# Kernel optimization log

Hardware: AMD Instinct MI355X
Metric: run time of the kernel (lower is better)

The kernel has to match this reference:

```python
import jax, jax.numpy as jnp
import numpy as np

B = 2048

def _conv(x, w, b, stride):
    y = jax.lax.conv_general_dilated(x, w, (stride, stride), 'VALID',
                                     dimension_numbers=('NCHW', 'OIHW', 'NCHW'))
    return y + b[None, :, None, None]

def _local_conv(x, w, b):
    # w: (Ho, Wo, Co, Ci, kh, kw), b: (Ho, Wo, Co); stride 1, valid
    Ho, Wo, Co, Ci, kh, kw = w.shape
    # patches: (B, Ci, kh*kw, Ho, Wo) -- sliding windows, small fixed loop over kernel taps
    patches = jnp.stack([x[:, :, i:i + Ho, j:j + Wo]
                         for i in range(kh) for j in range(kw)], axis=2)
    wf = w.reshape(Ho, Wo, Co, Ci, kh * kw)
    y = jnp.einsum('bcphw,hwocp->bohw', patches, wf)
    return y + jnp.transpose(b, (2, 0, 1))[None]

def setup_inputs() -> dict:
    key = jax.random.key(0)
    ks = jax.random.split(key, 18)
    s = 0.05
    inp = {
        'x': jax.random.normal(ks[0], (B, 5, 60, 60), dtype=jnp.float32),
        'info': jax.random.normal(ks[1], (B, 8), dtype=jnp.float32),
        'w1': jax.random.normal(ks[2], (32, 5, 3, 3), dtype=jnp.float32) * s,
        'b1': jnp.zeros((32,), dtype=jnp.float32),
        'w2a': jax.random.normal(ks[3], (64, 32, 3, 3), dtype=jnp.float32) * s,
        'b2a': jnp.zeros((64,), dtype=jnp.float32),
        'w2b': jax.random.normal(ks[4], (64, 64, 3, 3), dtype=jnp.float32) * s,
        'b2b': jnp.zeros((64,), dtype=jnp.float32),
        'lw3': jax.random.normal(ks[5], (9, 9, 64, 64, 5, 5), dtype=jnp.float32) * s,
        'lb3': jnp.zeros((9, 9, 64), dtype=jnp.float32),
        'lw4': jax.random.normal(ks[6], (5, 5, 64, 64, 5, 5), dtype=jnp.float32) * s,
        'lb4': jnp.zeros((5, 5, 64), dtype=jnp.float32),
        'lw5': jax.random.normal(ks[7], (3, 3, 64, 64, 3, 3), dtype=jnp.float32) * s,
        'lb5': jnp.zeros((3, 3, 64), dtype=jnp.float32),
        'hw': jax.random.normal(ks[8], (2, 584), dtype=jnp.float32) * s,
        'hb': jnp.zeros((2,), dtype=jnp.float32),
    }
    return inp

def reference(x, info, w1, b1, w2a, b2a, w2b, b2b, lw3, lb3, lw4, lb4, lw5, lb5, hw, hb):
    h = jnp.tanh(_conv(x, w1, b1, 2))            # (B,32,29,29)
    h = jnp.tanh(_conv(h, w2a, b2a, 1))          # (B,64,27,27)
    h = jnp.tanh(_conv(h, w2b, b2b, 2))          # (B,64,13,13)
    h = jnp.tanh(_local_conv(h, lw3, lb3))       # (B,64,9,9)
    h = jnp.tanh(_local_conv(h, lw4, lb4))       # (B,64,5,5)
    h = jnp.tanh(_local_conv(h, lw5, lb5))       # (B,64,3,3)
    h = h.reshape(h.shape[0], -1)                # (B,576)
    h = jnp.concatenate([h, info], axis=1)       # (B,584)
    logits = h @ hw.T + hb                       # (B,2)
    return jax.nn.softmax(logits, axis=1)
```

## Files before the change

### kernel.cpp

```cpp
#include <hip/hip_runtime.h>
#include <stdint.h>

#define THREADS 256

typedef short bf16x8 __attribute__((ext_vector_type(8)));
typedef float f32x4 __attribute__((ext_vector_type(4)));
typedef unsigned uint2_ __attribute__((ext_vector_type(2)));

__device__ __forceinline__ unsigned short f2bf(float v) {
  unsigned u = __builtin_bit_cast(unsigned, v);
  u = (u + 0x7fff + ((u >> 16) & 1)) >> 16;
  return (unsigned short)u;
}
__device__ __forceinline__ float bf2f(unsigned short h) {
  return __builtin_bit_cast(float, (unsigned)h << 16);
}
__device__ __forceinline__ float fast_tanh(float x) {
  return 1.f - 2.f / (__expf(2.f * x) + 1.f);
}

__device__ __forceinline__ int xcd_swizzle(int wg, int nwg) {
  const int q = nwg >> 3, rr = nwg & 7;
  const int xcd = wg & 7, l = wg >> 3;
  return (xcd < rr ? xcd * (q + 1) : rr * (q + 1) + (xcd - rr) * q) + l;
}

__global__ void pack_w1t(const float* __restrict__ w1, float* __restrict__ w1t) {
  int idx = blockIdx.x * THREADS + threadIdx.x;
  if (idx >= 45 * 32) return;
  int t = idx >> 5, co = idx & 31;
  w1t[t * 32 + co] = w1[co * 45 + t];
}

__global__ void __launch_bounds__(256) conv1_direct(
    const float* __restrict__ x, const float* __restrict__ w1t,
    const float* __restrict__ bias, unsigned short* __restrict__ out, int Bc,
    int bstart) {
  constexpr int CI = 5, CO = 32, IH = 60, IW = 60, OH = 29, OW = 29;
  constexpr int RPB = 2, NRB = 15;

  __shared__ float xs[CI * 5 * 60];

  const int tid = threadIdx.x;
  const int b = blockIdx.x / NRB;
  const int qb = blockIdx.x % NRB;
  const int oh0 = qb * RPB;
  const int rows = min(RPB, OH - oh0);
  const int ih0 = oh0 * 2;
  const int ihn = rows * 2 + 1;

  const float* xp = x + (size_t)(bstart + b) * (CI * IH * IW);

  const int nf4 = CI * ihn * 15;
  for (int i = tid; i < nf4; i += 256) {
    int col = i % 15;
    int row = i / 15;
    int ci = row / ihn, r = row % ihn;
    ((float4*)xs)[row * 15 + col] = ((const float4*)xp)[(ci * IH + ih0 + r) * 15 + col];
  }
  __syncthreads();

  const int lane = tid & 63;
  const int wu = __builtin_amdgcn_readfirstlane(tid >> 6);
  if (lane >= rows * OW) return;
  const int r = lane / OW, c = lane % OW;
  const int base = (r * 2) * 60 + c * 2;
  const int cstr = ihn * 60;

  float acc[8];
#pragma unroll
  for (int j = 0; j < 8; j++) acc[j] = bias[wu * 8 + j];

#pragma unroll
  for (int ci = 0; ci < CI; ci++)
#pragma unroll
    for (int kh = 0; kh < 3; kh++)
#pragma unroll
      for (int kw = 0; kw < 3; kw++) {
        const float v = xs[ci * cstr + base + kh * 60 + kw];
        const float* wt = w1t + ((ci * 3 + kh) * 3 + kw) * 32 + wu * 8;
#pragma unroll
        for (int j = 0; j < 8; j++) acc[j] = fmaf(v, wt[j], acc[j]);
      }

  const int p = (oh0 + r) * OW + c;
  bf16x8 o;
#pragma unroll
  for (int j = 0; j < 8; j++) o[j] = (short)f2bf(fast_tanh(acc[j]));
  *(bf16x8*)(out + ((size_t)p * Bc + b) * CO + wu * 8) = o;
}

template <int CI, int KS>
__global__ void __launch_bounds__(THREADS) pack_w(const float* __restrict__ w,
                                                  unsigned short* __restrict__ wp,
                                                  int npos) {
  constexpr int K = CI * KS * KS;
  constexpr int S = K / 32;
  int idx = blockIdx.x * THREADS + threadIdx.x;
  int total = npos * S * 2048;
  if (idx >= total) return;
  int e = idx & 7;
  int lane = (idx >> 3) & 63;
  int mt = (idx >> 9) & 3;
  int rest = idx >> 11;
  int s = rest % S, pos = rest / S;
  int co = mt * 16 + (lane & 15);
  int k = s * 32 + (lane >> 4) * 8 + e;
  int tap = k / CI, ci = k % CI;
  int kh = tap / KS, kw = tap % KS;
  float v = w[((((size_t)pos * 64 + co) * CI + ci) * KS + kh) * KS + kw];
  wp[idx] = f2bf(v);
}

template <int CI, int IH, int IW, int OH, int OW, int KS, int ST, bool LOCAL, int BW>
__global__ void __launch_bounds__(256) conv_mfma(
    const unsigned short* __restrict__ X, const unsigned short* __restrict__ Wp,
    const float* __restrict__ bias, unsigned short* __restrict__ Y, int Bc) {
  constexpr int S = CI * KS * KS / 32;
  constexpr int NPOS = OH * OW;
  constexpr int CW = 4 / BW;
  constexpr int MT = 4 / CW;

  const int tid = threadIdx.x;
  const int lane = tid & 63;
  const int wu = tid >> 6;
  const int n = lane & 15, g = lane >> 4;
  const int bw = wu % BW, cw = wu / BW;

  const int nbt = Bc / (BW * 64);
  int wg = xcd_swizzle(blockIdx.x, gridDim.x);
  int pos, btile;
  if (LOCAL) {
    btile = wg % nbt;
    pos = wg / nbt;
  } else {
    pos = wg % NPOS;
    btile = wg / NPOS;
  }
  const int oh = pos / OW, ow = pos % OW;
  const int b0 = btile * (BW * 64) + bw * 64;
  const int bA = b0 + n;

  const unsigned short* Wpp = Wp + (LOCAL ? (size_t)pos * (S * 2048) : 0);

  f32x4 acc[MT][4] = {};

#pragma unroll 2
  for (int s = 0; s < S; s++) {
    const int tap = (s * 32) / CI;
    const int ci0 = (s * 32) % CI + g * 8;
    const int kh = tap / KS, kw = tap % KS;
    const int pin = (oh * ST + kh) * IW + (ow * ST + kw);
    const unsigned short* xb = X + ((size_t)pin * Bc + bA) * CI + ci0;

    bf16x8 bfr[4];
#pragma unroll
    for (int j = 0; j < 4; j++) bfr[j] = *(const bf16x8*)(xb + j * 16 * CI);

    bf16x8 af[MT];
#pragma unroll
    for (int mt = 0; mt < MT; mt++)
      af[mt] =
          *(const bf16x8*)(Wpp + ((size_t)((s * 4 + cw * MT + mt) * 64 + lane) << 3));

#pragma unroll
    for (int mt = 0; mt < MT; mt++)
#pragma unroll
      for (int j = 0; j < 4; j++)
        acc[mt][j] =
            __builtin_amdgcn_mfma_f32_16x16x32_bf16(af[mt], bfr[j], acc[mt][j], 0, 0, 0);
  }

#pragma unroll
  for (int mt = 0; mt < MT; mt++) {
#pragma unroll
    for (int j = 0; j < 4; j++) {
      unsigned short o[4];
#pragma unroll
      for (int r = 0; r < 4; r++) {
        const int co = (cw * MT + mt) * 16 + g * 4 + r;
        o[r] = f2bf(fast_tanh(acc[mt][j][r] +
                              (LOCAL ? bias[pos * 64 + co] : bias[co])));
      }
      const int b = b0 + j * 16 + n;
      uint2_ pk;
      pk[0] = (unsigned)o[0] | ((unsigned)o[1] << 16);
      pk[1] = (unsigned)o[2] | ((unsigned)o[3] << 16);
      *(uint2_*)(Y + ((size_t)pos * Bc + b) * 64 + (cw * MT + mt) * 16 + g * 4) = pk;
    }
  }
}

__global__ void head_k(const unsigned short* __restrict__ h5,
                       const float* __restrict__ info, const float* __restrict__ hw,
                       const float* __restrict__ hb, float* __restrict__ out, int Bc,
                       int bstart) {
  int b = blockIdx.x * THREADS + threadIdx.x;
  if (b >= Bc) return;
  float l0 = hb[0], l1 = hb[1];
  for (int pos = 0; pos < 9; pos++) {
#pragma unroll
    for (int cb = 0; cb < 8; cb++) {
      bf16x8 v8 = *(const bf16x8*)(h5 + ((size_t)pos * Bc + b) * 64 + cb * 8);
#pragma unroll
      for (int j = 0; j < 8; j++) {
        float v = bf2f((unsigned short)v8[j]);
        int f = (cb * 8 + j) * 9 + pos;
        l0 = fmaf(v, hw[f], l0);
        l1 = fmaf(v, hw[584 + f], l1);
      }
    }
  }
#pragma unroll
  for (int k = 0; k < 8; k++) {
    float v = info[(size_t)(bstart + b) * 8 + k];
    l0 = fmaf(v, hw[576 + k], l0);
    l1 = fmaf(v, hw[584 + 576 + k], l1);
  }
  float m = fmaxf(l0, l1);
  float e0 = __expf(l0 - m), e1 = __expf(l1 - m);
  float s = e0 + e1;
  out[(size_t)(bstart + b) * 2 + 0] = e0 / s;
  out[(size_t)(bstart + b) * 2 + 1] = e1 / s;
}


extern "C" void kernel_launch(void* const* d_in, const int* in_sizes, int n_in,
                              void* d_out, int out_size, void* d_ws, size_t ws_size,
                              hipStream_t stream) {
  const float* x = (const float*)d_in[0];
  const float* info = (const float*)d_in[1];
  const float* w1 = (const float*)d_in[2];
  const float* b1 = (const float*)d_in[3];
  const float* w2a = (const float*)d_in[4];
  const float* b2a = (const float*)d_in[5];
  const float* w2b = (const float*)d_in[6];
  const float* b2b = (const float*)d_in[7];
  const float* lw3 = (const float*)d_in[8];
  const float* lb3 = (const float*)d_in[9];
  const float* lw4 = (const float*)d_in[10];
  const float* lb4 = (const float*)d_in[11];
  const float* lw5 = (const float*)d_in[12];
  const float* lb5 = (const float*)d_in[13];
  const float* hw = (const float*)d_in[14];
  const float* hb = (const float*)d_in[15];
  float* out = (float*)d_out;

  const int B = in_sizes[0] / 18000;

  const size_t SZ2A = 9ull * 2048, SZ2B = 18ull * 2048, SZ3 = 81ull * 50 * 2048,
               SZ4 = 25ull * 50 * 2048, SZ5 = 9ull * 18 * 2048;
  unsigned short* wp2a = (unsigned short*)d_ws;
  unsigned short* wp2b = wp2a + SZ2A;
  unsigned short* wp3 = wp2b + SZ2B;
  unsigned short* wp4 = wp3 + SZ3;
  unsigned short* wp5 = wp4 + SZ4;
  size_t wp_bytes = (SZ2A + SZ2B + SZ3 + SZ4 + SZ5) * 2;
  wp_bytes = (wp_bytes + 255) & ~(size_t)255;
  float* w1t = (float*)((char*)d_ws + wp_bytes);
  size_t w1t_bytes = ((45 * 32 * 4) + 255) & ~(size_t)255;

  const size_t PSA = 53824, PSB = 93312;
  const size_t per_sample = PSA + PSB;
  int Bc = B;
  while (Bc > 256 && wp_bytes + w1t_bytes + (size_t)Bc * per_sample + 4096 > ws_size)
    Bc >>= 1;

  char* base = (char*)d_ws + wp_bytes + w1t_bytes;
  unsigned short* bufA = (unsigned short*)base;
  unsigned short* bufB = (unsigned short*)(base + (size_t)Bc * PSA);

  hipLaunchKernelGGL(pack_w1t, dim3(6), dim3(THREADS), 0, stream, w1, w1t);
  hipLaunchKernelGGL((pack_w<32, 3>), dim3((SZ2A + 255) / 256), dim3(THREADS), 0, stream,
                     w2a, wp2a, 1);
  hipLaunchKernelGGL((pack_w<64, 3>), dim3((SZ2B + 255) / 256), dim3(THREADS), 0, stream,
                     w2b, wp2b, 1);
  hipLaunchKernelGGL((pack_w<64, 5>), dim3((SZ3 + 255) / 256), dim3(THREADS), 0, stream,
                     lw3, wp3, 81);
  hipLaunchKernelGGL((pack_w<64, 5>), dim3((SZ4 + 255) / 256), dim3(THREADS), 0, stream,
                     lw4, wp4, 25);
  hipLaunchKernelGGL((pack_w<64, 3>), dim3((SZ5 + 255) / 256), dim3(THREADS), 0, stream,
                     lw5, wp5, 9);

  const int nchunks = B / Bc;
  for (int c = 0; c < nchunks; c++) {
    const int bstart = c * Bc;

    hipLaunchKernelGGL(conv1_direct, dim3(Bc * 15), dim3(256), 0, stream, x, w1t, b1,
                       bufA, Bc, bstart);
    hipLaunchKernelGGL((conv_mfma<32, 29, 29, 27, 27, 3, 1, false, 4>),
                       dim3(729 * (Bc / 256)), dim3(256), 0, stream, bufA, wp2a, b2a,
                       bufB, Bc);
    hipLaunchKernelGGL((conv_mfma<64, 27, 27, 13, 13, 3, 2, false, 4>),
                       dim3(169 * (Bc / 256)), dim3(256), 0, stream, bufB, wp2b, b2b,
                       bufA, Bc);
    hipLaunchKernelGGL((conv_mfma<64, 13, 13, 9, 9, 5, 1, true, 4>),
                       dim3(81 * (Bc / 256)), dim3(256), 0, stream, bufA, wp3, lb3, bufB,
                       Bc);
    hipLaunchKernelGGL((conv_mfma<64, 9, 9, 5, 5, 5, 1, true, 2>),
                       dim3(25 * (Bc / 128)), dim3(256), 0, stream, bufB, wp4, lb4, bufA,
                       Bc);
    hipLaunchKernelGGL((conv_mfma<64, 5, 5, 3, 3, 3, 1, true, 1>),
                       dim3(9 * (Bc / 64)), dim3(256), 0, stream, bufA, wp5, lb5, bufB,
                       Bc);
    hipLaunchKernelGGL(head_k, dim3((Bc + THREADS - 1) / THREADS), dim3(THREADS), 0,
                       stream, bufB, info, hw, hb, out, Bc, bstart);
  }
}
```

Baseline: 640.7 us.

## Retile MFMA conv warp tiles and double-buffer fragment loads across K steps

Generalises the conv_mfma warp tile to MT=BW co-tiles by NJ batch subtiles, and retunes per-layer tiles. Dense convs use 2x8 tiles per wave (more reuse of weights across batch) and the local convs use smaller batch tiles, which gives more workgroups. The K loop now prefetches the next step's A/B fragments into a second register set before issuing MFMAs on the current one, overlapping global loads with compute. This raises register pressure, and the smaller local-conv tiles reload weights more often.

```diff
diff --git a/kernel.cpp b/kernel.cpp
--- a/kernel.cpp
+++ b/kernel.cpp
@@ -112,14 +112,15 @@
   wp[idx] = f2bf(v);
 }
 
-template <int CI, int IH, int IW, int OH, int OW, int KS, int ST, bool LOCAL, int BW>
+template <int CI, int IH, int IW, int OH, int OW, int KS, int ST, bool LOCAL, int BW,
+          int NJ>
 __global__ void __launch_bounds__(256) conv_mfma(
     const unsigned short* __restrict__ X, const unsigned short* __restrict__ Wp,
     const float* __restrict__ bias, unsigned short* __restrict__ Y, int Bc) {
   constexpr int S = CI * KS * KS / 32;
   constexpr int NPOS = OH * OW;
-  constexpr int CW = 4 / BW;
-  constexpr int MT = 4 / CW;
+  constexpr int MT = BW;
+  constexpr int BPB = BW * NJ * 16;
 
   const int tid = threadIdx.x;
   const int lane = tid & 63;
@@ -127,7 +128,7 @@
   const int n = lane & 15, g = lane >> 4;
   const int bw = wu % BW, cw = wu / BW;
 
-  const int nbt = Bc / (BW * 64);
+  const int nbt = Bc / BPB;
   int wg = xcd_swizzle(blockIdx.x, gridDim.x);
   int pos, btile;
   if (LOCAL) {
@@ -138,43 +139,48 @@
     btile = wg / NPOS;
   }
   const int oh = pos / OW, ow = pos % OW;
-  const int b0 = btile * (BW * 64) + bw * 64;
+  const int b0 = btile * BPB + bw * (NJ * 16);
   const int bA = b0 + n;
 
   const unsigned short* Wpp = Wp + (LOCAL ? (size_t)pos * (S * 2048) : 0);
 
-  f32x4 acc[MT][4] = {};
-
-#pragma unroll 2
-  for (int s = 0; s < S; s++) {
+  auto LD = [&](int s, bf16x8* af, bf16x8* bf) {
     const int tap = (s * 32) / CI;
     const int ci0 = (s * 32) % CI + g * 8;
     const int kh = tap / KS, kw = tap % KS;
     const int pin = (oh * ST + kh) * IW + (ow * ST + kw);
     const unsigned short* xb = X + ((size_t)pin * Bc + bA) * CI + ci0;
-
-    bf16x8 bfr[4];
-#pragma unroll
-    for (int j = 0; j < 4; j++) bfr[j] = *(const bf16x8*)(xb + j * 16 * CI);
-
-    bf16x8 af[MT];
+#pragma unroll
+    for (int j = 0; j < NJ; j++) bf[j] = *(const bf16x8*)(xb + j * 16 * CI);
 #pragma unroll
     for (int mt = 0; mt < MT; mt++)
       af[mt] =
           *(const bf16x8*)(Wpp + ((size_t)((s * 4 + cw * MT + mt) * 64 + lane) << 3));
-
+  };
+
+  f32x4 acc[MT][NJ] = {};
+  auto MM = [&](bf16x8* af, bf16x8* bf) {
 #pragma unroll
     for (int mt = 0; mt < MT; mt++)
 #pragma unroll
-      for (int j = 0; j < 4; j++)
+      for (int j = 0; j < NJ; j++)
         acc[mt][j] =
-            __builtin_amdgcn_mfma_f32_16x16x32_bf16(af[mt], bfr[j], acc[mt][j], 0, 0, 0);
+            __builtin_amdgcn_mfma_f32_16x16x32_bf16(af[mt], bf[j], acc[mt][j], 0, 0, 0);
+  };
+
+  bf16x8 afA[MT], bfA[NJ], afB[MT], bfB[NJ];
+  LD(0, afA, bfA);
+  for (int s = 0; s < S; s += 2) {
+    if (s + 1 < S) LD(s + 1, afB, bfB);
+    MM(afA, bfA);
+    if (s + 2 < S) LD(s + 2, afA, bfA);
+    if (s + 1 < S) MM(afB, bfB);
   }
 
 #pragma unroll
   for (int mt = 0; mt < MT; mt++) {
 #pragma unroll
-    for (int j = 0; j < 4; j++) {
+    for (int j = 0; j < NJ; j++) {
       unsigned short o[4];
 #pragma unroll
       for (int r = 0; r < 4; r++) {
@@ -288,20 +294,20 @@
 
     hipLaunchKernelGGL(conv1_direct, dim3(Bc * 15), dim3(256), 0, stream, x, w1t, b1,
                        bufA, Bc, bstart);
-    hipLaunchKernelGGL((conv_mfma<32, 29, 29, 27, 27, 3, 1, false, 4>),
+    hipLaunchKernelGGL((conv_mfma<32, 29, 29, 27, 27, 3, 1, false, 2, 8>),
                        dim3(729 * (Bc / 256)), dim3(256), 0, stream, bufA, wp2a, b2a,
                        bufB, Bc);
-    hipLaunchKernelGGL((conv_mfma<64, 27, 27, 13, 13, 3, 2, false, 4>),
+    hipLaunchKernelGGL((conv_mfma<64, 27, 27, 13, 13, 3, 2, false, 2, 8>),
                        dim3(169 * (Bc / 256)), dim3(256), 0, stream, bufB, wp2b, b2b,
                        bufA, Bc);
-    hipLaunchKernelGGL((conv_mfma<64, 13, 13, 9, 9, 5, 1, true, 4>),
-                       dim3(81 * (Bc / 256)), dim3(256), 0, stream, bufA, wp3, lb3, bufB,
+    hipLaunchKernelGGL((conv_mfma<64, 13, 13, 9, 9, 5, 1, true, 2, 4>),
+                       dim3(81 * (Bc / 128)), dim3(256), 0, stream, bufA, wp3, lb3, bufB,
                        Bc);
-    hipLaunchKernelGGL((conv_mfma<64, 9, 9, 5, 5, 5, 1, true, 2>),
-                       dim3(25 * (Bc / 128)), dim3(256), 0, stream, bufB, wp4, lb4, bufA,
+    hipLaunchKernelGGL((conv_mfma<64, 9, 9, 5, 5, 5, 1, true, 1, 4>),
+                       dim3(25 * (Bc / 64)), dim3(256), 0, stream, bufB, wp4, lb4, bufA,
                        Bc);
-    hipLaunchKernelGGL((conv_mfma<64, 5, 5, 3, 3, 3, 1, true, 1>),
-                       dim3(9 * (Bc / 64)), dim3(256), 0, stream, bufA, wp5, lb5, bufB,
+    hipLaunchKernelGGL((conv_mfma<64, 5, 5, 3, 3, 3, 1, true, 1, 2>),
+                       dim3(9 * (Bc / 32)), dim3(256), 0, stream, bufA, wp5, lb5, bufB,
                        Bc);
     hipLaunchKernelGGL(head_k, dim3((Bc + THREADS - 1) / THREADS), dim3(THREADS), 0,
                        stream, bufB, info, hw, hb, out, Bc, bstart);
```

Measured after the change: 737.0 us. +15.0%, slower.

## Stage conv MFMA operands through double-buffered LDS with async global-to-LDS loads

Applied to the files above, without the earlier changes.

The MFMA conv kernel now stages each K-slice of packed weights and activations into shared memory using global_load_lds, double-buffered so the next slice loads while the current one is multiplied. Every wave now covers all 64 output channels over its own batch sub-tile, so weights are fetched once per block instead of per wave. The last local conv now uses 128-sample tiles. The change adds one barrier per K step and more LDS use, and the 16-byte global_load_lds width depends on hardware support.

```diff
diff --git a/kernel.cpp b/kernel.cpp
--- a/kernel.cpp
+++ b/kernel.cpp
@@ -6,6 +6,9 @@
 typedef short bf16x8 __attribute__((ext_vector_type(8)));
 typedef float f32x4 __attribute__((ext_vector_type(4)));
 typedef unsigned uint2_ __attribute__((ext_vector_type(2)));
+
+#define GPTR(x) ((const __attribute__((address_space(1))) void*)(x))
+#define LPTR(x) ((__attribute__((address_space(3))) void*)(x))
 
 __device__ __forceinline__ unsigned short f2bf(float v) {
   unsigned u = __builtin_bit_cast(unsigned, v);
@@ -112,22 +115,24 @@
   wp[idx] = f2bf(v);
 }
 
-template <int CI, int IH, int IW, int OH, int OW, int KS, int ST, bool LOCAL, int BW>
+template <int CI, int IH, int IW, int OH, int OW, int KS, int ST, bool LOCAL, int BT>
 __global__ void __launch_bounds__(256) conv_mfma(
     const unsigned short* __restrict__ X, const unsigned short* __restrict__ Wp,
     const float* __restrict__ bias, unsigned short* __restrict__ Y, int Bc) {
   constexpr int S = CI * KS * KS / 32;
   constexpr int NPOS = OH * OW;
-  constexpr int CW = 4 / BW;
-  constexpr int MT = 4 / CW;
+  constexpr int NJ = BT / 64;
+  constexpr int NB = BT / 64;
+
+  __shared__ unsigned short As[2][2048];
+  __shared__ unsigned short Bs[2][BT * 32];
 
   const int tid = threadIdx.x;
   const int lane = tid & 63;
   const int wu = tid >> 6;
   const int n = lane & 15, g = lane >> 4;
-  const int bw = wu % BW, cw = wu / BW;
-
-  const int nbt = Bc / (BW * 64);
+
+  const int nbt = Bc / BT;
   int wg = xcd_swizzle(blockIdx.x, gridDim.x);
   int pos, btile;
   if (LOCAL) {
@@ -138,55 +143,72 @@
     btile = wg / NPOS;
   }
   const int oh = pos / OW, ow = pos % OW;
-  const int b0 = btile * (BW * 64) + bw * 64;
-  const int bA = b0 + n;
+  const int b0 = btile * BT;
 
   const unsigned short* Wpp = Wp + (LOCAL ? (size_t)pos * (S * 2048) : 0);
 
-  f32x4 acc[MT][4] = {};
-
-#pragma unroll 2
-  for (int s = 0; s < S; s++) {
+  const int srow = tid >> 2;
+  const int scol = (tid & 3) * 8;
+
+  auto stage = [&](int s, int buf) {
+    __builtin_amdgcn_global_load_lds(GPTR(Wpp + s * 2048 + tid * 8),
+                                     LPTR(&As[buf][tid * 8]), 16, 0, 0);
     const int tap = (s * 32) / CI;
-    const int ci0 = (s * 32) % CI + g * 8;
+    const int ci0 = (s * 32) % CI;
     const int kh = tap / KS, kw = tap % KS;
     const int pin = (oh * ST + kh) * IW + (ow * ST + kw);
-    const unsigned short* xb = X + ((size_t)pin * Bc + bA) * CI + ci0;
-
-    bf16x8 bfr[4];
-#pragma unroll
-    for (int j = 0; j < 4; j++) bfr[j] = *(const bf16x8*)(xb + j * 16 * CI);
-
-    bf16x8 af[MT];
-#pragma unroll
-    for (int mt = 0; mt < MT; mt++)
-      af[mt] =
-          *(const bf16x8*)(Wpp + ((size_t)((s * 4 + cw * MT + mt) * 64 + lane) << 3));
-
-#pragma unroll
-    for (int mt = 0; mt < MT; mt++)
-#pragma unroll
-      for (int j = 0; j < 4; j++)
+    const size_t base = (size_t)pin * Bc + b0;
+#pragma unroll
+    for (int i = 0; i < NB; i++)
+      __builtin_amdgcn_global_load_lds(
+          GPTR(X + (base + i * 64 + srow) * CI + ci0 + scol),
+          LPTR(&Bs[buf][i * 2048 + tid * 8]), 16, 0, 0);
+  };
+
+  f32x4 acc[4][NJ] = {};
+
+  stage(0, 0);
+  int buf = 0;
+  for (int s = 0; s < S; s++) {
+    __syncthreads();
+    if (s + 1 < S) stage(s + 1, buf ^ 1);
+
+    bf16x8 bfr[NJ];
+#pragma unroll
+    for (int j = 0; j < NJ; j++) {
+      const int local_b = wu * (NJ * 16) + j * 16 + n;
+      bfr[j] = *(const bf16x8*)(&Bs[buf][local_b * 32 + g * 8]);
+    }
+    bf16x8 af[4];
+#pragma unroll
+    for (int mt = 0; mt < 4; mt++)
+      af[mt] = *(const bf16x8*)(&As[buf][(mt * 64 + lane) * 8]);
+
+#pragma unroll
+    for (int mt = 0; mt < 4; mt++)
+#pragma unroll
+      for (int j = 0; j < NJ; j++)
         acc[mt][j] =
             __builtin_amdgcn_mfma_f32_16x16x32_bf16(af[mt], bfr[j], acc[mt][j], 0, 0, 0);
-  }
-
-#pragma unroll
-  for (int mt = 0; mt < MT; mt++) {
-#pragma unroll
-    for (int j = 0; j < 4; j++) {
+    buf ^= 1;
+  }
+
+#pragma unroll
+  for (int mt = 0; mt < 4; mt++) {
+#pragma unroll
+    for (int j = 0; j < NJ; j++) {
       unsigned short o[4];
 #pragma unroll
       for (int r = 0; r < 4; r++) {
-        const int co = (cw * MT + mt) * 16 + g * 4 + r;
+        const int co = mt * 16 + g * 4 + r;
         o[r] = f2bf(fast_tanh(acc[mt][j][r] +
                               (LOCAL ? bias[pos * 64 + co] : bias[co])));
       }
-      const int b = b0 + j * 16 + n;
+      const int b = b0 + wu * (NJ * 16) + j * 16 + n;
       uint2_ pk;
       pk[0] = (unsigned)o[0] | ((unsigned)o[1] << 16);
       pk[1] = (unsigned)o[2] | ((unsigned)o[3] << 16);
-      *(uint2_*)(Y + ((size_t)pos * Bc + b) * 64 + (cw * MT + mt) * 16 + g * 4) = pk;
+      *(uint2_*)(Y + ((size_t)pos * Bc + b) * 64 + mt * 16 + g * 4) = pk;
     }
   }
 }
@@ -288,20 +310,20 @@
 
     hipLaunchKernelGGL(conv1_direct, dim3(Bc * 15), dim3(256), 0, stream, x, w1t, b1,
                        bufA, Bc, bstart);
-    hipLaunchKernelGGL((conv_mfma<32, 29, 29, 27, 27, 3, 1, false, 4>),
+    hipLaunchKernelGGL((conv_mfma<32, 29, 29, 27, 27, 3, 1, false, 256>),
                        dim3(729 * (Bc / 256)), dim3(256), 0, stream, bufA, wp2a, b2a,
                        bufB, Bc);
-    hipLaunchKernelGGL((conv_mfma<64, 27, 27, 13, 13, 3, 2, false, 4>),
+    hipLaunchKernelGGL((conv_mfma<64, 27, 27, 13, 13, 3, 2, false, 256>),
                        dim3(169 * (Bc / 256)), dim3(256), 0, stream, bufB, wp2b, b2b,
                        bufA, Bc);
-    hipLaunchKernelGGL((conv_mfma<64, 13, 13, 9, 9, 5, 1, true, 4>),
+    hipLaunchKernelGGL((conv_mfma<64, 13, 13, 9, 9, 5, 1, true, 256>),
                        dim3(81 * (Bc / 256)), dim3(256), 0, stream, bufA, wp3, lb3, bufB,
                        Bc);
-    hipLaunchKernelGGL((conv_mfma<64, 9, 9, 5, 5, 5, 1, true, 2>),
+    hipLaunchKernelGGL((conv_mfma<64, 9, 9, 5, 5, 5, 1, true, 128>),
                        dim3(25 * (Bc / 128)), dim3(256), 0, stream, bufB, wp4, lb4, bufA,
                        Bc);
-    hipLaunchKernelGGL((conv_mfma<64, 5, 5, 3, 3, 3, 1, true, 1>),
-                       dim3(9 * (Bc / 64)), dim3(256), 0, stream, bufA, wp5, lb5, bufB,
+    hipLaunchKernelGGL((conv_mfma<64, 5, 5, 3, 3, 3, 1, true, 128>),
+                       dim3(9 * (Bc / 128)), dim3(256), 0, stream, bufA, wp5, lb5, bufB,
                        Bc);
     hipLaunchKernelGGL(head_k, dim3((Bc + THREADS - 1) / THREADS), dim3(THREADS), 0,
                        stream, bufB, info, hw, hb, out, Bc, bstart);
```

Measured after the change: 537.6 us. -16.1%, faster.
